# Performance work log

Hardware: AMD Instinct MI355X
Metric: run time of the kernel (lower is better)

Reference implementation:

```python
import jax, jax.numpy as jnp
import numpy as np

D_MODEL = 1024
N_HEADS = 16
HEAD_DIM = D_MODEL // N_HEADS


def setup_inputs() -> dict:
    key = jax.random.key(0)
    k1, k2, k3 = jax.random.split(key, 3)
    x = jax.random.normal(k1, (4, 2048, D_MODEL), dtype=jnp.float32)
    w_qkv = jax.random.normal(k2, (D_MODEL, 3 * D_MODEL), dtype=jnp.float32) * (D_MODEL ** -0.5)
    w_proj = jax.random.normal(k3, (D_MODEL, D_MODEL), dtype=jnp.float32) * (D_MODEL ** -0.5)
    return {"x": x, "w_qkv": w_qkv, "w_proj": w_proj}


def reference(x, w_qkv, w_proj):
    B, T, C = x.shape
    qkv = x @ w_qkv                      # [B,T,3C]
    q, k, v = jnp.split(qkv, 3, axis=-1)
    # [B,T,H,Dh] -> [B,H,T,Dh]
    q = q.reshape(B, T, N_HEADS, HEAD_DIM).transpose(0, 2, 1, 3)
    k = k.reshape(B, T, N_HEADS, HEAD_DIM).transpose(0, 2, 1, 3)
    v = v.reshape(B, T, N_HEADS, HEAD_DIM).transpose(0, 2, 1, 3)
    scale = 1.0 / jnp.sqrt(jnp.asarray(HEAD_DIM, dtype=x.dtype))
    attn = jnp.einsum('bhqd,bhkd->bhqk', q, k) * scale   # [B,H,T,T]
    causal = jnp.tril(jnp.ones((T, T), dtype=bool))
    attn = jnp.where(causal[None, None], attn, jnp.asarray(-jnp.inf, dtype=attn.dtype))
    attn = jax.nn.softmax(attn, axis=-1)
    out = jnp.einsum('bhqk,bhkd->bhqd', attn, v)          # [B,H,T,Dh]
    out = out.transpose(0, 2, 1, 3).reshape(B, T, C)
    return out @ w_proj
```

## Files before the change

kernel.cpp:

```cpp
#include <hip/hip_runtime.h>
#include <hip/hip_bf16.h>
#include <stdint.h>

#define D_MODEL 1024
#define N_HEADS 16
#define HEAD_DIM 64
#define B_SZ 4
#define T_SEQ 2048
#define BH_TOT (B_SZ * N_HEADS)
#define M_ROWS (B_SZ * T_SEQ)

typedef float floatx4 __attribute__((ext_vector_type(4)));
typedef __bf16 bf16x8 __attribute__((ext_vector_type(8)));

#if __has_builtin(__builtin_amdgcn_exp2f)
#define EXP2(x) __builtin_amdgcn_exp2f(x)
#else
#define EXP2(x) exp2f(x)
#endif

__device__ inline unsigned short f2bf(float f) {
  union { float f; unsigned int u; } c; c.f = f;
  unsigned int u = c.u;
  unsigned int r = (u + 0x7FFFu + ((u >> 16) & 1u)) >> 16;
  return (unsigned short)r;
}

__device__ inline unsigned short bfc(float f) {
  return __builtin_bit_cast(unsigned short, (__bf16)f);
}

__device__ inline unsigned int pk2(float lo, float hi) {
  return (unsigned int)bfc(lo) | ((unsigned int)bfc(hi) << 16);
}

__device__ __forceinline__ void gload16(const unsigned short* g,
                                        unsigned short* l) {
  __builtin_amdgcn_global_load_lds(
      (const __attribute__((address_space(1))) void*)g,
      (__attribute__((address_space(3))) void*)l, 16, 0, 0);
}

__global__ void cvt_f32_bf16(const float* __restrict__ in,
                             unsigned short* __restrict__ out, int n) {
  int i = (blockIdx.x * blockDim.x + threadIdx.x) * 4;
  if (i + 3 < n) {
    float4 v = *(const float4*)(in + i);
    out[i + 0] = f2bf(v.x);
    out[i + 1] = f2bf(v.y);
    out[i + 2] = f2bf(v.z);
    out[i + 3] = f2bf(v.w);
  } else {
    for (; i < n; ++i) out[i] = f2bf(in[i]);
  }
}

__global__ __launch_bounds__(256) void cvt_transpose(
    const float* __restrict__ in, unsigned short* __restrict__ out,
    int K, int N) {
  __shared__ unsigned short tile[32][33];
  const int n0 = blockIdx.x * 32;
  const int k0 = blockIdx.y * 32;
  const int tx = threadIdx.x & 31;
  const int ty = threadIdx.x >> 5;
#pragma unroll
  for (int r = ty; r < 32; r += 8)
    tile[r][tx] = f2bf(in[(size_t)(k0 + r) * N + n0 + tx]);
  __syncthreads();
#pragma unroll
  for (int r = ty; r < 32; r += 8)
    out[(size_t)(n0 + r) * K + k0 + tx] = tile[tx][r];
}

#define QSCALE 0.1803368801111204f
template <int EPI>
__global__ __launch_bounds__(256) void gemm_bf16(
    const unsigned short* __restrict__ A,
    const unsigned short* __restrict__ Bt, int M, int N, int K,
    unsigned short* __restrict__ Qb, unsigned short* __restrict__ Kb,
    unsigned short* __restrict__ Vt, float* __restrict__ Cout) {
  const int bn = blockIdx.x * 128;
  const int bm = blockIdx.y * 128;
  const int tid = threadIdx.x;
  const int lane = tid & 63;
  const int w = tid >> 6;
  const int wr = w >> 1, wc = w & 1;
  const int l15 = lane & 15;
  const int lg = lane >> 4;
  const int l7 = l15 & 7;

  __shared__ unsigned short As[128 * 64];
  __shared__ unsigned short Bs[128 * 64];

  floatx4 acc[4][4] = {};

  const int srl = lane >> 3;
  const int ssw = ((lane & 7) ^ srl) * 8;

  for (int k0 = 0; k0 < K; k0 += 64) {
#pragma unroll
    for (int p2 = 0; p2 < 4; ++p2) {
      const int rbase = p2 * 32 + w * 8;
      gload16(&A[(size_t)(bm + rbase + srl) * K + k0 + ssw], &As[rbase * 64]);
      gload16(&Bt[(size_t)(bn + rbase + srl) * K + k0 + ssw], &Bs[rbase * 64]);
    }
    __syncthreads();

#pragma unroll
    for (int kk = 0; kk < 2; ++kk) {
      bf16x8 af[4], bfr[4];
#pragma unroll
      for (int mt = 0; mt < 4; ++mt)
        af[mt] = *(const bf16x8*)&As[(wr * 64 + mt * 16 + l15) * 64 +
                                     (((kk * 4 + lg) ^ l7) << 3)];
#pragma unroll
      for (int nt = 0; nt < 4; ++nt)
        bfr[nt] = *(const bf16x8*)&Bs[(wc * 64 + nt * 16 + l15) * 64 +
                                      (((kk * 4 + lg) ^ l7) << 3)];
#pragma unroll
      for (int mt = 0; mt < 4; ++mt)
#pragma unroll
        for (int nt = 0; nt < 4; ++nt)
          acc[mt][nt] = __builtin_amdgcn_mfma_f32_16x16x32_bf16(
              af[mt], bfr[nt], acc[mt][nt], 0, 0, 0);
    }
    __syncthreads();
  }

#pragma unroll
  for (int mt = 0; mt < 4; ++mt)
#pragma unroll
    for (int nt = 0; nt < 4; ++nt) {
      const int n = bn + wc * 64 + nt * 16 + l15;
      const int m0 = bm + wr * 64 + mt * 16 + lg * 4;
      if (EPI == 0 && (n >> 10) == 2) {
        int b = m0 >> 11;
        int t = m0 & (T_SEQ - 1);
        int nn = n & (D_MODEL - 1);
        int h = nn >> 6;
        int dh = nn & 63;
        ushort4 v4;
        v4.x = bfc(acc[mt][nt][0]);
        v4.y = bfc(acc[mt][nt][1]);
        v4.z = bfc(acc[mt][nt][2]);
        v4.w = bfc(acc[mt][nt][3]);
        *(ushort4*)&Vt[((size_t)((b * N_HEADS + h) * HEAD_DIM) + dh) * T_SEQ +
                       t] = v4;
      } else {
#pragma unroll
        for (int i = 0; i < 4; ++i) {
          int m = m0 + i;
          float v = acc[mt][nt][i];
          if (EPI == 0) {
            int b = m >> 11;
            int t = m & (T_SEQ - 1);
            int part = n >> 10;
            int nn = n & (D_MODEL - 1);
            int h = nn >> 6;
            int dh = nn & 63;
            size_t idx =
                ((size_t)(b * N_HEADS + h) * T_SEQ + t) * HEAD_DIM + dh;
            if (part == 0)
              Qb[idx] = bfc(v * QSCALE);
            else
              Kb[idx] = bfc(v);
          } else {
            Cout[(size_t)m * N + n] = v;
          }
        }
      }
    }
}

__global__ __launch_bounds__(256) void attn_fwd(
    const unsigned short* __restrict__ Qb, const unsigned short* __restrict__ Kb,
    const unsigned short* __restrict__ Vt, unsigned short* __restrict__ Ob) {
  const int head = blockIdx.x;
  const int p = blockIdx.y;
  const int tid = threadIdx.x;
  const int wid = tid >> 6;
  const int lane = tid & 63;
  const int l15 = lane & 15;
  const int lg = lane >> 4;
  const int l7 = l15 & 7;
  const int b = head >> 4;
  const int h = head & 15;

  const unsigned short* Qh = Qb + (size_t)head * T_SEQ * HEAD_DIM;
  const unsigned short* Kh = Kb + (size_t)head * T_SEQ * HEAD_DIM;
  const unsigned short* Vh = Vt + (size_t)head * HEAD_DIM * T_SEQ;

  __shared__ unsigned short Ks[2][64 * 64];
  __shared__ unsigned short Vs[2][64 * 64];
  __shared__ unsigned short Ps[4 * 2 * 16 * 64];

  const int swz8 = (((lane & 7) ^ (lane >> 3)) << 3);
  const int srow = wid * 16 + (lane >> 3);
  const size_t kLane0 = (size_t)srow * HEAD_DIM + swz8;
  const size_t kLane1 = (size_t)(srow + 8) * HEAD_DIM + swz8;
  const size_t vLane0 = (size_t)srow * T_SEQ + swz8;
  const size_t vLane1 = (size_t)(srow + 8) * T_SEQ + swz8;
  const int ldsW = wid * 1024;

  int kfo0[4], kfo1[4], vfo[2][4];
#pragma unroll
  for (int c = 0; c < 4; ++c) {
    kfo0[c] = (c * 16 + l15) * 64 + ((lg ^ l7) << 3);
    kfo1[c] = (c * 16 + l15) * 64 + (((4 + lg) ^ l7) << 3);
  }
#pragma unroll
  for (int kc = 0; kc < 2; ++kc)
#pragma unroll
    for (int d = 0; d < 4; ++d)
      vfo[kc][d] = (d * 16 + l15) * 64 + (((kc * 4 + lg) ^ l7) << 3);
  int pwo[4];
#pragma unroll
  for (int c = 0; c < 4; ++c)
    pwo[c] = l15 * 64 + (((2 * c + (lg >> 1)) ^ l7) << 3) + (lg & 1) * 4;
  const int pro0 = l15 * 64 + ((lg ^ l7) << 3);
  const int pro1 = l15 * 64 + (((4 + lg) ^ l7) << 3);

  for (int ph = 0; ph < 2; ++ph) {
    const int rbase = (ph == 0) ? p * 128 : 2048 - 128 * (p + 1);
    const int nst = (ph == 0) ? 2 * p + 2 : 32 - 2 * p;
    const int q0 = rbase + wid * 32;

    bf16x8 qf[2][2];
#pragma unroll
    for (int t = 0; t < 2; ++t)
#pragma unroll
      for (int c = 0; c < 2; ++c)
        qf[t][c] = *(const bf16x8*)&Qh[(size_t)(q0 + t * 16 + l15) * 64 +
                                       c * 32 + lg * 8];

    floatx4 o[2][4] = {};
    float m_run[2] = {-1e30f, -1e30f};
    float l_part[2] = {0.f, 0.f};

    __syncthreads();
    gload16(Kh + kLane0, &Ks[0][ldsW]);
    gload16(Kh + kLane1, &Ks[0][ldsW + 512]);
    gload16(Vh + vLane0, &Vs[0][ldsW]);
    gload16(Vh + vLane1, &Vs[0][ldsW + 512]);

    int cur = 0;
    for (int kb = 0; kb < nst; ++kb, cur ^= 1) {
      const int kbase = kb * 64;
      __syncthreads();

      if (kb + 1 < nst) {
        const size_t ko = (size_t)(kbase + 64) * HEAD_DIM;
        const int vo = kbase + 64;
        gload16(Kh + ko + kLane0, &Ks[cur ^ 1][ldsW]);
        gload16(Kh + ko + kLane1, &Ks[cur ^ 1][ldsW + 512]);
        gload16(Vh + vo + vLane0, &Vs[cur ^ 1][ldsW]);
        gload16(Vh + vo + vLane1, &Vs[cur ^ 1][ldsW + 512]);
      }

      if (kbase <= q0 + 31) {
        const unsigned short* Kc = Ks[cur];
        const unsigned short* Vc = Vs[cur];
        bf16x8 kf0[4], kf1[4];
#pragma unroll
        for (int c = 0; c < 4; ++c) {
          kf0[c] = *(const bf16x8*)&Kc[kfo0[c]];
          kf1[c] = *(const bf16x8*)&Kc[kfo1[c]];
        }
        bf16x8 vf[2][4];
#pragma unroll
        for (int kc = 0; kc < 2; ++kc)
#pragma unroll
          for (int d = 0; d < 4; ++d) vf[kc][d] = *(const bf16x8*)&Vc[vfo[kc][d]];

        floatx4 st_[2][4] = {};
        __builtin_amdgcn_s_setprio(1);
#pragma unroll
        for (int c = 0; c < 4; ++c) {
          st_[0][c] = __builtin_amdgcn_mfma_f32_16x16x32_bf16(kf0[c], qf[0][0], st_[0][c], 0, 0, 0);
          st_[0][c] = __builtin_amdgcn_mfma_f32_16x16x32_bf16(kf1[c], qf[0][1], st_[0][c], 0, 0, 0);
          st_[1][c] = __builtin_amdgcn_mfma_f32_16x16x32_bf16(kf0[c], qf[1][0], st_[1][c], 0, 0, 0);
          st_[1][c] = __builtin_amdgcn_mfma_f32_16x16x32_bf16(kf1[c], qf[1][1], st_[1][c], 0, 0, 0);
        }
        __builtin_amdgcn_s_setprio(0);

        if (kbase + 63 > q0) {
#pragma unroll
          for (int t = 0; t < 2; ++t) {
            const int thr = q0 + t * 16 + l15 - kbase;
#pragma unroll
            for (int c = 0; c < 4; ++c)
#pragma unroll
              for (int i = 0; i < 4; ++i)
                if (c * 16 + lg * 4 + i > thr) st_[t][c][i] = -1e30f;
          }
        }

        float lmax[2];
        bool need = false;
#pragma unroll
        for (int t = 0; t < 2; ++t) {
          float v0 = fmaxf(fmaxf(st_[t][0][0], st_[t][0][1]),
                           fmaxf(st_[t][0][2], st_[t][0][3]));
          float v1 = fmaxf(fmaxf(st_[t][1][0], st_[t][1][1]),
                           fmaxf(st_[t][1][2], st_[t][1][3]));
          float v2 = fmaxf(fmaxf(st_[t][2][0], st_[t][2][1]),
                           fmaxf(st_[t][2][2], st_[t][2][3]));
          float v3 = fmaxf(fmaxf(st_[t][3][0], st_[t][3][1]),
                           fmaxf(st_[t][3][2], st_[t][3][3]));
          lmax[t] = fmaxf(fmaxf(v0, v1), fmaxf(v2, v3));
          need |= (lmax[t] > m_run[t] + 8.0f);
        }
        if (__any(need)) {
#pragma unroll
          for (int t = 0; t < 2; ++t) {
            float pm = lmax[t];
            pm = fmaxf(pm, __shfl_xor(pm, 16));
            pm = fmaxf(pm, __shfl_xor(pm, 32));
            float mnew = fmaxf(m_run[t], pm);
            float alpha = EXP2(m_run[t] - mnew);
            m_run[t] = mnew;
            l_part[t] *= alpha;
#pragma unroll
            for (int c = 0; c < 4; ++c) o[t][c] *= alpha;
          }
        }

#pragma unroll
        for (int t = 0; t < 2; ++t) {
          const int tb = (wid * 2 + t) * 1024;
          float sum = 0.f;
#pragma unroll
          for (int c = 0; c < 4; ++c) {
#pragma unroll
            for (int i = 0; i < 4; ++i) {
              st_[t][c][i] = EXP2(st_[t][c][i] - m_run[t]);
              sum += st_[t][c][i];
            }
            uint2 wv;
            wv.x = pk2(st_[t][c][0], st_[t][c][1]);
            wv.y = pk2(st_[t][c][2], st_[t][c][3]);
            *(uint2*)&Ps[tb + pwo[c]] = wv;
          }
          l_part[t] += sum;
        }

        __builtin_amdgcn_s_setprio(1);
#pragma unroll
        for (int t = 0; t < 2; ++t) {
          const int tb = (wid * 2 + t) * 1024;
          bf16x8 pb0 = *(const bf16x8*)&Ps[tb + pro0];
          bf16x8 pb1 = *(const bf16x8*)&Ps[tb + pro1];
#pragma unroll
          for (int dt = 0; dt < 4; ++dt) {
            o[t][dt] = __builtin_amdgcn_mfma_f32_16x16x32_bf16(vf[0][dt], pb0, o[t][dt], 0, 0, 0);
            o[t][dt] = __builtin_amdgcn_mfma_f32_16x16x32_bf16(vf[1][dt], pb1, o[t][dt], 0, 0, 0);
          }
        }
        __builtin_amdgcn_s_setprio(0);
      }
    }

#pragma unroll
    for (int t = 0; t < 2; ++t) {
      float l = l_part[t];
      l += __shfl_xor(l, 16);
      l += __shfl_xor(l, 32);
      float inv = 1.0f / l;
      int q = q0 + t * 16 + l15;
      size_t base = ((size_t)(b * T_SEQ + q)) * D_MODEL + h * HEAD_DIM;
#pragma unroll
      for (int dt = 0; dt < 4; ++dt) {
        unsigned int u0 = pk2(o[t][dt][0] * inv, o[t][dt][1] * inv);
        unsigned int u1 = pk2(o[t][dt][2] * inv, o[t][dt][3] * inv);
        *(unsigned int*)&Ob[base + dt * 16 + lg * 4] = u0;
        *(unsigned int*)&Ob[base + dt * 16 + lg * 4 + 2] = u1;
      }
    }
  }
}

extern "C" void kernel_launch(void* const* d_in, const int* in_sizes, int n_in,
                              void* d_out, int out_size, void* d_ws,
                              size_t ws_size, hipStream_t stream) {
  const float* x = (const float*)d_in[0];
  const float* w_qkv = (const float*)d_in[1];
  const float* w_proj = (const float*)d_in[2];
  float* out = (float*)d_out;

  char* ws = (char*)d_ws;
  size_t off = 0;
  unsigned short* x_bf = (unsigned short*)(ws + off);
  off += (size_t)M_ROWS * D_MODEL * 2;
  unsigned short* wqkv_t = (unsigned short*)(ws + off);
  off += (size_t)D_MODEL * 3 * D_MODEL * 2;
  unsigned short* wproj_t = (unsigned short*)(ws + off);
  off += (size_t)D_MODEL * D_MODEL * 2;
  unsigned short* Qb = (unsigned short*)(ws + off);
  off += (size_t)BH_TOT * T_SEQ * HEAD_DIM * 2;
  unsigned short* Kb = (unsigned short*)(ws + off);
  off += (size_t)BH_TOT * T_SEQ * HEAD_DIM * 2;
  unsigned short* Vt = (unsigned short*)(ws + off);
  off += (size_t)BH_TOT * T_SEQ * HEAD_DIM * 2;
  unsigned short* Ob = (unsigned short*)(ws + off);
  off += (size_t)M_ROWS * D_MODEL * 2;

  int n1 = M_ROWS * D_MODEL;
  cvt_f32_bf16<<<(n1 / 4 + 255) / 256, 256, 0, stream>>>(x, x_bf, n1);
  cvt_transpose<<<dim3(3 * D_MODEL / 32, D_MODEL / 32), 256, 0, stream>>>(
      w_qkv, wqkv_t, D_MODEL, 3 * D_MODEL);
  cvt_transpose<<<dim3(D_MODEL / 32, D_MODEL / 32), 256, 0, stream>>>(
      w_proj, wproj_t, D_MODEL, D_MODEL);

  gemm_bf16<0><<<dim3(3 * D_MODEL / 128, M_ROWS / 128), 256, 0, stream>>>(
      x_bf, wqkv_t, M_ROWS, 3 * D_MODEL, D_MODEL, Qb, Kb, Vt, nullptr);

  attn_fwd<<<dim3(BH_TOT, 8), 256, 0, stream>>>(Qb, Kb, Vt, Ob);

  gemm_bf16<1><<<dim3(D_MODEL / 128, M_ROWS / 128), 256, 0, stream>>>(
      Ob, wproj_t, M_ROWS, D_MODEL, D_MODEL, nullptr, nullptr, nullptr, out);
}
```

Measured before the change: 187.7 us.

## Stage two 64-key sub-tiles per barrier and shrink per-wave P scratch

The attention loop now loads 128 keys (two 64-row K/V sub-tiles) per double-buffer stage, which halves the number of __syncthreads barriers and global-load issue points per query block. Each sub-tile is processed in turn inside the stage, with the causal skip applied per sub-tile. The P scratch buffer shrinks to one 16x64 tile per wave and is reused per query sub-row: it is written, read back, and consumed by the PV MFMA before the next row. This frees LDS for the doubled K/V buffers. In exchange, LDS per block rises, which can reduce occupancy, and the reuse serializes P writes and reads within each wave.

```diff
diff --git a/kernel.cpp b/kernel.cpp
--- a/kernel.cpp
+++ b/kernel.cpp
@@ -190,9 +190,9 @@
   const unsigned short* Kh = Kb + (size_t)head * T_SEQ * HEAD_DIM;
   const unsigned short* Vh = Vt + (size_t)head * HEAD_DIM * T_SEQ;
 
-  __shared__ unsigned short Ks[2][64 * 64];
-  __shared__ unsigned short Vs[2][64 * 64];
-  __shared__ unsigned short Ps[4 * 2 * 16 * 64];
+  __shared__ unsigned short Ks[2][2][64 * 64];
+  __shared__ unsigned short Vs[2][2][64 * 64];
+  __shared__ unsigned short Ps[4 * 16 * 64];
 
   const int swz8 = (((lane & 7) ^ (lane >> 3)) << 3);
   const int srow = wid * 16 + (lane >> 3);
@@ -222,7 +222,7 @@
 
   for (int ph = 0; ph < 2; ++ph) {
     const int rbase = (ph == 0) ? p * 128 : 2048 - 128 * (p + 1);
-    const int nst = (ph == 0) ? 2 * p + 2 : 32 - 2 * p;
+    const int nst = (ph == 0) ? p + 1 : 16 - p;
     const int q0 = rbase + wid * 32;
 
     bf16x8 qf[2][2];
@@ -238,28 +238,39 @@
     float l_part[2] = {0.f, 0.f};
 
     __syncthreads();
-    gload16(Kh + kLane0, &Ks[0][ldsW]);
-    gload16(Kh + kLane1, &Ks[0][ldsW + 512]);
-    gload16(Vh + vLane0, &Vs[0][ldsW]);
-    gload16(Vh + vLane1, &Vs[0][ldsW + 512]);
+#pragma unroll
+    for (int s = 0; s < 2; ++s) {
+      const size_t ko = (size_t)(s * 64) * HEAD_DIM;
+      gload16(Kh + ko + kLane0, &Ks[0][s][ldsW]);
+      gload16(Kh + ko + kLane1, &Ks[0][s][ldsW + 512]);
+      gload16(Vh + s * 64 + vLane0, &Vs[0][s][ldsW]);
+      gload16(Vh + s * 64 + vLane1, &Vs[0][s][ldsW + 512]);
+    }
 
     int cur = 0;
     for (int kb = 0; kb < nst; ++kb, cur ^= 1) {
-      const int kbase = kb * 64;
+      const int kb128 = kb * 128;
       __syncthreads();
 
       if (kb + 1 < nst) {
-        const size_t ko = (size_t)(kbase + 64) * HEAD_DIM;
-        const int vo = kbase + 64;
-        gload16(Kh + ko + kLane0, &Ks[cur ^ 1][ldsW]);
-        gload16(Kh + ko + kLane1, &Ks[cur ^ 1][ldsW + 512]);
-        gload16(Vh + vo + vLane0, &Vs[cur ^ 1][ldsW]);
-        gload16(Vh + vo + vLane1, &Vs[cur ^ 1][ldsW + 512]);
+#pragma unroll
+        for (int s = 0; s < 2; ++s) {
+          const size_t ko = (size_t)(kb128 + 128 + s * 64) * HEAD_DIM;
+          const int vo = kb128 + 128 + s * 64;
+          gload16(Kh + ko + kLane0, &Ks[cur ^ 1][s][ldsW]);
+          gload16(Kh + ko + kLane1, &Ks[cur ^ 1][s][ldsW + 512]);
+          gload16(Vh + vo + vLane0, &Vs[cur ^ 1][s][ldsW]);
+          gload16(Vh + vo + vLane1, &Vs[cur ^ 1][s][ldsW + 512]);
+        }
       }
 
-      if (kbase <= q0 + 31) {
-        const unsigned short* Kc = Ks[cur];
-        const unsigned short* Vc = Vs[cur];
+#pragma unroll
+      for (int sub = 0; sub < 2; ++sub) {
+        const int kbase = kb128 + sub * 64;
+        if (kbase > q0 + 31) continue;
+
+        const unsigned short* Kc = Ks[cur][sub];
+        const unsigned short* Vc = Vs[cur][sub];
         bf16x8 kf0[4], kf1[4];
 #pragma unroll
         for (int c = 0; c < 4; ++c) {
@@ -327,7 +338,6 @@
 
 #pragma unroll
         for (int t = 0; t < 2; ++t) {
-          const int tb = (wid * 2 + t) * 1024;
           float sum = 0.f;
 #pragma unroll
           for (int c = 0; c < 4; ++c) {
@@ -339,24 +349,20 @@
             uint2 wv;
             wv.x = pk2(st_[t][c][0], st_[t][c][1]);
             wv.y = pk2(st_[t][c][2], st_[t][c][3]);
-            *(uint2*)&Ps[tb + pwo[c]] = wv;
+            *(uint2*)&Ps[ldsW + pwo[c]] = wv;
           }
           l_part[t] += sum;
-        }
-
-        __builtin_amdgcn_s_setprio(1);
-#pragma unroll
-        for (int t = 0; t < 2; ++t) {
-          const int tb = (wid * 2 + t) * 1024;
-          bf16x8 pb0 = *(const bf16x8*)&Ps[tb + pro0];
-          bf16x8 pb1 = *(const bf16x8*)&Ps[tb + pro1];
+
+          bf16x8 pb0 = *(const bf16x8*)&Ps[ldsW + pro0];
+          bf16x8 pb1 = *(const bf16x8*)&Ps[ldsW + pro1];
+          __builtin_amdgcn_s_setprio(1);
 #pragma unroll
           for (int dt = 0; dt < 4; ++dt) {
             o[t][dt] = __builtin_amdgcn_mfma_f32_16x16x32_bf16(vf[0][dt], pb0, o[t][dt], 0, 0, 0);
             o[t][dt] = __builtin_amdgcn_mfma_f32_16x16x32_bf16(vf[1][dt], pb1, o[t][dt], 0, 0, 0);
           }
-        }
-        __builtin_amdgcn_s_setprio(0);
+          __builtin_amdgcn_s_setprio(0);
+        }
       }
     }
 
```

Result: slower. 210.4 us (+12.1%).
